# Performance work log

Measured on AMD Instinct MI355X. Metric: run time of the kernel, lower is better.

Reference implementation:

```python
import jax, jax.numpy as jnp
import numpy as np

N, E, L, F, M = 512, 2048, 16, 16, 8
HOPS = 2      # egonet radius (k_hop_subgraph num_hops)
H = 128       # WL hash buckets
N_ITER = 3    # WeisfeilerLehman(n_iter=3)
TAU = 0.1     # soft-relabeling temperature


def setup_inputs():
    key = jax.random.key(0)
    k0, k1, k2, k3, k4, k5 = jax.random.split(key, 6)
    labels = jax.random.randint(k0, (N,), 0, L)
    x = jax.nn.one_hot(labels, L, dtype=jnp.float32)
    edge_index = jax.random.randint(k1, (2, E), 0, N)
    # filter adjacencies, built exactly as in GKernel.__init__:
    # symmetric 0/1 with zero diagonal
    A = jax.random.uniform(k2, (F, M, M))
    A = ((A + jnp.swapaxes(A, -1, -2)) > 1.0).astype(jnp.float32)
    A = A * (1.0 - jnp.eye(M, dtype=jnp.float32))
    Xlab = jax.random.randint(k3, (F, M), 0, L)
    X = jax.nn.one_hot(Xlab, L, dtype=jnp.float32)
    # injective label -> bucket embedding (random distinct buckets)
    E0 = jax.nn.one_hot(jax.random.permutation(k4, H)[:L], H, dtype=jnp.float32)
    # random projection used to hash (own-label, neighbor-multiset) signatures
    Rproj = jax.random.normal(k5, (2 * H, H), dtype=jnp.float32)
    return {"x": x, "edge_index": edge_index, "P": A, "X": X, "E0": E0, "Rproj": Rproj}


def _wl_features(c0, nbr_sum, mask, Rproj):
    # soft Weisfeiler-Lehman subtree features: at each iteration the new
    # node label is a hash of (own label, neighbor-label multiset); the
    # graph feature is the concatenated per-iteration label histograms.
    c = c0 * mask[:, None]                       # [n, H]
    feats = [c.sum(0)]
    for _ in range(N_ITER):
        sig = jnp.concatenate([c, nbr_sum(c)], axis=-1)        # [n, 2H]
        c = jax.nn.softmax((sig @ Rproj) / TAU, axis=-1) * mask[:, None]
        feats.append(c.sum(0))
    return jnp.concatenate(feats)                # [(N_ITER+1)*H]


def _max_comp_mask(A):
    # largest connected component via min-label propagation (max_comp)
    comp = jnp.arange(M, dtype=jnp.float32)
    Ab = A > 0
    for _ in range(M):
        nbr_min = jnp.min(jnp.where(Ab, comp[None, :], 1e9), axis=1)
        comp = jnp.minimum(comp, nbr_min)
    ci = comp.astype(jnp.int32)
    counts = jax.ops.segment_sum(jnp.ones(M, jnp.float32), ci, num_segments=M)
    best = jnp.argmax(counts)
    return (ci == best).astype(jnp.float32)


def reference(x, edge_index, P, X, E0, Rproj):
    # symmetrize edges (egonets / WL kernels are undirected)
    src = jnp.concatenate([edge_index[0], edge_index[1]])
    dst = jnp.concatenate([edge_index[1], edge_index[0]])
    # --- k-hop egonet node masks (compute_egonets) : reach[i, j] = 1 iff
    # node j is within HOPS hops of root i ---
    reach = jnp.eye(N, dtype=jnp.float32)
    for _ in range(HOPS):
        agg = jax.ops.segment_sum(reach[:, src].T, dst, num_segments=N).T
        reach = jnp.clip(reach + agg, 0.0, 1.0)
    c0 = x @ E0                                  # initial bucket labels [N, H]

    def ego_feat(mask):
        emask = (mask[src] * mask[dst])[:, None]
        def nbr(c):
            return jax.ops.segment_sum(c[src] * emask, dst, num_segments=N)
        return _wl_features(c0, nbr, mask, Rproj)

    ego_feats = jax.vmap(ego_feat)(reach)        # [N, (N_ITER+1)*H]

    def filt_feat(Af, Xf):
        mask = _max_comp_mask(Af)
        Am = Af * mask[:, None] * mask[None, :]
        return _wl_features(Xf @ E0, lambda c: Am @ c, mask, Rproj)

    filt_feats = jax.vmap(filt_feat)(P, X)       # [F, (N_ITER+1)*H]

    # normalized WL kernel: k(g1,g2)/sqrt(k(g1,g1) k(g2,g2)); sim.T -> [N, F]
    sim = filt_feats @ ego_feats.T               # [F, N]
    nf = jnp.linalg.norm(filt_feats, axis=-1)
    ng = jnp.linalg.norm(ego_feats, axis=-1)
    sim = sim / (nf[:, None] * ng[None, :] + 1e-12)
    return sim.T
```

## Files before the change

kernel.cpp:

```cpp
#include <hip/hip_runtime.h>
#include <hip/hip_bf16.h>

#define NN 512
#define EE 2048
#define LL 16
#define FF 16
#define MM 8
#define HH 128
#define CAP_ROWS 40960
#define MAXD 32
#define TAU_SCALE 14.426950408889634f

typedef __attribute__((ext_vector_type(8))) short bf16x8;
typedef __attribute__((ext_vector_type(4))) float f32x4;

constexpr size_t OFF_ADJ   = 0;
constexpr size_t SZ_ADJ    = (size_t)NN * 8 * 8;
constexpr size_t OFF_DEG   = OFF_ADJ + SZ_ADJ;
constexpr size_t SZ_DEG    = (size_t)NN * 4;
constexpr size_t OFF_CNT   = OFF_DEG + SZ_DEG;
constexpr size_t SZ_CNT    = (size_t)NN * 4;
constexpr size_t OFF_ROFF  = OFF_CNT + SZ_CNT;
constexpr size_t SZ_ROFF   = (size_t)(NN + 1) * 4 + 12;
constexpr size_t OFF_BUCKN = OFF_ROFF + SZ_ROFF;
constexpr size_t SZ_BUCKN  = (size_t)NN * 4;
constexpr size_t OFF_BUCKF = OFF_BUCKN + SZ_BUCKN;
constexpr size_t SZ_BUCKF  = (size_t)FF * MM * 4;
constexpr size_t OFF_NLST  = ((OFF_BUCKF + SZ_BUCKF + 63) / 64) * 64;
constexpr size_t SZ_NLST   = (size_t)NN * MAXD * 2;
constexpr size_t OFF_CEGO  = OFF_NLST + SZ_NLST;
constexpr size_t SZ_CEGO   = (size_t)CAP_ROWS * 2;
constexpr size_t OFF_NCNT  = OFF_CEGO + SZ_CEGO;
constexpr size_t SZ_NCNT   = (size_t)CAP_ROWS * 2;
constexpr size_t OFF_RBK   = OFF_NCNT + SZ_NCNT;
constexpr size_t SZ_RBK    = (size_t)CAP_ROWS * 2;
constexpr size_t OFF_NBR   = OFF_RBK + SZ_RBK;
constexpr size_t SZ_NBR    = (size_t)CAP_ROWS * MAXD * 2;
constexpr size_t OFF_NBK   = OFF_NBR + SZ_NBR;
constexpr size_t SZ_NBK    = (size_t)CAP_ROWS * MAXD * 2;
constexpr size_t OFF_EGOF  = ((OFF_NBK + SZ_NBK + 63) / 64) * 64;
constexpr size_t SZ_EGOF   = (size_t)NN * 512 * 4;
constexpr size_t OFF_FILTF = OFF_EGOF + SZ_EGOF;
constexpr size_t SZ_FILTF  = (size_t)FF * 512 * 4;
constexpr size_t OFF_FNORM = OFF_FILTF + SZ_FILTF;
constexpr size_t SZ_FNORM  = 64;
constexpr size_t OFF_CA    = ((OFF_FNORM + SZ_FNORM + 255) / 256) * 256;
constexpr size_t SZ_CBUF   = (size_t)CAP_ROWS * HH * 4;
constexpr size_t OFF_CB    = OFF_CA + SZ_CBUF;

__device__ __forceinline__ unsigned f2bfbits(float x) {
    unsigned u = __float_as_uint(x);
    return (u + 0x7fffu + ((u >> 16) & 1u)) >> 16;
}
__device__ __forceinline__ float bf2f(unsigned hb) { return __uint_as_float(hb << 16); }

__global__ __launch_bounds__(256) void k_build(const int* __restrict__ ei,
                                               const float* __restrict__ x,
                                               const float* __restrict__ X,
                                               const float* __restrict__ E0,
                                               int* __restrict__ degN,
                                               unsigned short* __restrict__ nbrLstN,
                                               unsigned long long* __restrict__ adj,
                                               int* __restrict__ buckN,
                                               int* __restrict__ buckF) {
    int idx = blockIdx.x * blockDim.x + threadIdx.x;
    if (idx < EE) {
        int a = ei[idx], b = ei[EE + idx];
        int p = atomicAdd(&degN[a], 1);
        if (p < MAXD) nbrLstN[(size_t)a * MAXD + p] = (unsigned short)b;
        int q = atomicAdd(&degN[b], 1);
        if (q < MAXD) nbrLstN[(size_t)b * MAXD + q] = (unsigned short)a;
        atomicOr(&adj[(size_t)a * 8 + (b >> 6)], 1ull << (b & 63));
        atomicOr(&adj[(size_t)b * 8 + (a >> 6)], 1ull << (a & 63));
    } else if (idx < EE + NN) {
        int i = idx - EE;
        int lab = 0;
        for (int l = 0; l < LL; ++l) if (x[i * LL + l] > 0.5f) lab = l;
        int b = 0;
        for (int h = 0; h < HH; ++h) if (E0[lab * HH + h] > 0.5f) b = h;
        buckN[i] = b;
    } else if (idx < EE + NN + FF * MM) {
        int fm = idx - EE - NN;
        int lab = 0;
        for (int l = 0; l < LL; ++l) if (X[fm * LL + l] > 0.5f) lab = l;
        int b = 0;
        for (int h = 0; h < HH; ++h) if (E0[lab * HH + h] > 0.5f) b = h;
        buckF[fm] = b;
    }
}

__global__ __launch_bounds__(64) void k_reach(const unsigned long long* __restrict__ adj,
                                              unsigned long long* __restrict__ bitsR,
                                              int* __restrict__ count) {
    __shared__ unsigned long long r1[8];
    __shared__ unsigned long long r2[8];
    int i = blockIdx.x, t = threadIdx.x;
    if (t < 8) {
        unsigned long long v = adj[(size_t)i * 8 + t];
        if (t == (i >> 6)) v |= 1ull << (i & 63);
        r1[t] = v;
        r2[t] = v;
    }
    __syncthreads();
    unsigned long long p[8] = {0, 0, 0, 0, 0, 0, 0, 0};
    for (int rep = 0; rep < 8; ++rep) {
        if ((r1[rep] >> t) & 1ull) {
            int j = t + rep * 64;
#pragma unroll
            for (int w = 0; w < 8; ++w) p[w] |= adj[(size_t)j * 8 + w];
        }
    }
#pragma unroll
    for (int w = 0; w < 8; ++w)
        if (p[w]) atomicOr(&r2[w], p[w]);
    __syncthreads();
    if (t < 8) bitsR[(size_t)i * 8 + t] = r2[t];
    if (t == 0) {
        int acc = 0;
        for (int w = 0; w < 8; ++w) acc += __popcll(r2[w]);
        count[i] = acc;
    }
}

__global__ __launch_bounds__(512) void k_scan(const int* __restrict__ in,
                                              int* __restrict__ out) {
    __shared__ int s[NN];
    int t = threadIdx.x;
    s[t] = in[t];
    __syncthreads();
    for (int d = 1; d < NN; d <<= 1) {
        int v = (t >= d) ? s[t - d] : 0;
        __syncthreads();
        s[t] += v;
        __syncthreads();
    }
    out[t + 1] = s[t];
    if (t == 0) out[0] = 0;
}

__global__ __launch_bounds__(64) void k_pack(const unsigned long long* __restrict__ bitsR,
                                             const int* __restrict__ count,
                                             const int* __restrict__ rowOff,
                                             const int* __restrict__ degN,
                                             const unsigned short* __restrict__ nbrLstN,
                                             const int* __restrict__ buckN,
                                             unsigned short* __restrict__ nbrRow,
                                             unsigned short* __restrict__ nbrBuck,
                                             unsigned short* __restrict__ nbrCnt,
                                             unsigned short* __restrict__ rowBuck,
                                             unsigned short* __restrict__ cegoG,
                                             float* __restrict__ egoF) {
    __shared__ unsigned long long bits[8];
    __shared__ int wpre[8];
    __shared__ unsigned short cmap_s[NN];
    __shared__ unsigned short nodes_s[NN];
    __shared__ float f0[HH];
    int i = blockIdx.x, t = threadIdx.x;
    if (t < 8) bits[t] = bitsR[(size_t)i * 8 + t];
    if (t < 64) { f0[t] = 0.0f; f0[t + 64] = 0.0f; }
    __syncthreads();
    if (t == 0) {
        int acc = 0;
        for (int w = 0; w < 8; ++w) { wpre[w] = acc; acc += __popcll(bits[w]); }
    }
    __syncthreads();
    int base = rowOff[i];
    int n = count[i];
    if (base >= CAP_ROWS) n = 0;
    else if (base + n > CAP_ROWS) n = CAP_ROWS - base;
    for (int rep = 0; rep < 8; ++rep) {
        int j = t + rep * 64;
        unsigned long long word = bits[rep];
        unsigned short v = 0xFFFFu;
        if ((word >> t) & 1ull) {
            int idx = wpre[rep] + __popcll(word & ((1ull << t) - 1ull));
            if (idx < n) { v = (unsigned short)idx; nodes_s[idx] = (unsigned short)j; }
        }
        cmap_s[j] = v;
    }
    for (int q = 256 + t; q < 512; q += 64) egoF[(size_t)i * 512 + q] = 0.0f;
    __syncthreads();
    for (int m = t; m < n; m += 64) {
        int j = nodes_s[m];
        int b = buckN[j];
        atomicAdd(&f0[b], 1.0f);
        size_t row = (size_t)(base + m);
        rowBuck[row] = (unsigned short)b;
        int dn = degN[j]; if (dn > MAXD) dn = MAXD;
        int cnt = 0;
        for (int e = 0; e < dn; ++e) {
            unsigned short nbNode = nbrLstN[(size_t)j * MAXD + e];
            unsigned short nr = cmap_s[nbNode];
            if (nr != 0xFFFFu && cnt < MAXD) {
                nbrRow[row * MAXD + cnt] = (unsigned short)(base + nr);
                nbrBuck[row * MAXD + cnt] = (unsigned short)buckN[nbNode];
                cnt++;
            }
        }
        nbrCnt[row] = (unsigned short)cnt;
        cegoG[row] = (unsigned short)i;
    }
    __syncthreads();
    if (t < 64) {
        egoF[(size_t)i * 512 + t] = f0[t];
        egoF[(size_t)i * 512 + t + 64] = f0[t + 64];
    }
}

__global__ __launch_bounds__(256) void k_iter1(const int* __restrict__ count,
                                               const int* __restrict__ rowOff,
                                               const unsigned short* __restrict__ rowBuck,
                                               const unsigned short* __restrict__ nbrBuck,
                                               const unsigned short* __restrict__ nbrCnt,
                                               const float* __restrict__ Rg,
                                               float* __restrict__ cOut,
                                               float* __restrict__ egoF) {
    __shared__ float fs[HH];
    int i = blockIdx.x, tid = threadIdx.x;
    int base = rowOff[i];
    int n = count[i];
    if (base >= CAP_ROWS) n = 0;
    else if (base + n > CAP_ROWS) n = CAP_ROWS - base;
    if (tid < HH) fs[tid] = 0.0f;
    __syncthreads();
    const float* Rb = Rg + (size_t)HH * HH;
    int col = (tid & 7) * 16;
    float facc[16];
#pragma unroll
    for (int q = 0; q < 16; ++q) facc[q] = 0.0f;
    for (int m = tid >> 3; m < n; m += 32) {
        int gr = base + m;
        float z[16];
        const float* rt = Rg + (size_t)rowBuck[gr] * HH + col;
#pragma unroll
        for (int q = 0; q < 4; ++q) *(float4*)&z[q * 4] = *(const float4*)&rt[q * 4];
        int cnt = nbrCnt[gr];
        const unsigned short* nk = &nbrBuck[(size_t)gr * MAXD];
        for (int e = 0; e < cnt; ++e) {
            const float* rb = Rb + (size_t)nk[e] * HH + col;
#pragma unroll
            for (int q = 0; q < 4; ++q) {
                float4 rv = *(const float4*)&rb[q * 4];
                z[q * 4 + 0] += rv.x; z[q * 4 + 1] += rv.y;
                z[q * 4 + 2] += rv.z; z[q * 4 + 3] += rv.w;
            }
        }
        float mx = z[0];
#pragma unroll
        for (int q = 1; q < 16; ++q) mx = fmaxf(mx, z[q]);
        for (int off = 4; off > 0; off >>= 1) mx = fmaxf(mx, __shfl_xor(mx, off));
        float s = 0.0f;
#pragma unroll
        for (int q = 0; q < 16; ++q) { z[q] = exp2f((z[q] - mx) * TAU_SCALE); s += z[q]; }
        for (int off = 4; off > 0; off >>= 1) s += __shfl_xor(s, off);
        float inv = 1.0f / s;
        float* crow = cOut + (size_t)gr * HH + col;
#pragma unroll
        for (int q = 0; q < 16; ++q) { z[q] *= inv; facc[q] += z[q]; }
#pragma unroll
        for (int q = 0; q < 4; ++q) *(float4*)&crow[q * 4] = *(const float4*)&z[q * 4];
    }
#pragma unroll
    for (int q = 0; q < 16; ++q) atomicAdd(&fs[col + q], facc[q]);
    __syncthreads();
    if (tid < HH) egoF[(size_t)i * 512 + HH + tid] = fs[tid];
}

__global__ __launch_bounds__(256) void k_prep(const float* __restrict__ Rg,
                                              short* __restrict__ RtH,
                                              short* __restrict__ RtL) {
    int idx = blockIdx.x * blockDim.x + threadIdx.x;
    int col = idx >> 5;
    int kc = (idx & 31) * 8;
    bf16x8 hv, lv;
#pragma unroll
    for (int j = 0; j < 8; ++j) {
        float xv = Rg[(size_t)(kc + j) * HH + col];
        unsigned hb = f2bfbits(xv);
        hv[j] = (short)hb;
        lv[j] = (short)f2bfbits(xv - bf2f(hb));
    }
    *(bf16x8*)&RtH[(size_t)col * 256 + kc] = hv;
    *(bf16x8*)&RtL[(size_t)col * 256 + kc] = lv;
}

__global__ __launch_bounds__(64) void k_iter(const float* __restrict__ cur,
                                             float* __restrict__ nxt,
                                             const short* __restrict__ RtH,
                                             const short* __restrict__ RtL,
                                             const int* __restrict__ rowOff,
                                             const unsigned short* __restrict__ nbrRow,
                                             const unsigned short* __restrict__ nbrCnt,
                                             const unsigned short* __restrict__ cegoG,
                                             float* __restrict__ egoF,
                                             int it) {
    int Rtot = rowOff[NN];
    if (Rtot > CAP_ROWS) Rtot = CAP_ROWS;
    int r0 = blockIdx.x * 16;
    if (r0 >= Rtot) return;
    int tid = threadIdx.x;
    int c16 = tid & 15, g = tid >> 4;
    int kb = g * 8;
    int grA = r0 + c16;
    if (grA >= Rtot) grA = Rtot - 1;

    float ua[4][8];
#pragma unroll
    for (int s = 0; s < 4; ++s)
#pragma unroll
        for (int j = 0; j < 8; ++j) ua[s][j] = 0.0f;
    {
        int cnt = nbrCnt[grA];
        const unsigned short* nb = &nbrRow[(size_t)grA * MAXD];
        for (int e = 0; e < cnt; ++e) {
            const float* cr = &cur[(size_t)nb[e] * HH + kb];
#pragma unroll
            for (int s = 0; s < 4; ++s) {
                float4 v0 = *(const float4*)&cr[s * 32];
                float4 v1 = *(const float4*)&cr[s * 32 + 4];
                ua[s][0] += v0.x; ua[s][1] += v0.y; ua[s][2] += v0.z; ua[s][3] += v0.w;
                ua[s][4] += v1.x; ua[s][5] += v1.y; ua[s][6] += v1.z; ua[s][7] += v1.w;
            }
        }
    }

    f32x4 acc[8];
#pragma unroll
    for (int n = 0; n < 8; ++n) acc[n] = (f32x4)(0.0f);
    const short* bbH = RtH + (size_t)c16 * 256 + kb;
    const short* bbL = RtL + (size_t)c16 * 256 + kb;

#pragma unroll
    for (int s = 0; s < 4; ++s) {
        bf16x8 ahi, alo;
#pragma unroll
        for (int j = 0; j < 8; ++j) {
            float xv = ua[s][j];
            unsigned hb = f2bfbits(xv);
            ahi[j] = (short)hb;
            alo[j] = (short)f2bfbits(xv - bf2f(hb));
        }
        const int t = s + 4;
#pragma unroll
        for (int n = 0; n < 8; ++n) {
            bf16x8 bh = *(const bf16x8*)&bbH[n * 4096 + t * 32];
            bf16x8 bl = *(const bf16x8*)&bbL[n * 4096 + t * 32];
            acc[n] = __builtin_amdgcn_mfma_f32_16x16x32_bf16(ahi, bh, acc[n], 0, 0, 0);
            acc[n] = __builtin_amdgcn_mfma_f32_16x16x32_bf16(ahi, bl, acc[n], 0, 0, 0);
            acc[n] = __builtin_amdgcn_mfma_f32_16x16x32_bf16(alo, bh, acc[n], 0, 0, 0);
        }
    }
    {
        const float* cr = &cur[(size_t)grA * HH + kb];
#pragma unroll
        for (int t = 0; t < 4; ++t) {
            float4 v0 = *(const float4*)&cr[t * 32];
            float4 v1 = *(const float4*)&cr[t * 32 + 4];
            float cv[8] = {v0.x, v0.y, v0.z, v0.w, v1.x, v1.y, v1.z, v1.w};
            bf16x8 ahi, alo;
#pragma unroll
            for (int j = 0; j < 8; ++j) {
                unsigned hb = f2bfbits(cv[j]);
                ahi[j] = (short)hb;
                alo[j] = (short)f2bfbits(cv[j] - bf2f(hb));
            }
#pragma unroll
            for (int n = 0; n < 8; ++n) {
                bf16x8 bh = *(const bf16x8*)&bbH[n * 4096 + t * 32];
                bf16x8 bl = *(const bf16x8*)&bbL[n * 4096 + t * 32];
                acc[n] = __builtin_amdgcn_mfma_f32_16x16x32_bf16(ahi, bh, acc[n], 0, 0, 0);
                acc[n] = __builtin_amdgcn_mfma_f32_16x16x32_bf16(ahi, bl, acc[n], 0, 0, 0);
                acc[n] = __builtin_amdgcn_mfma_f32_16x16x32_bf16(alo, bh, acc[n], 0, 0, 0);
            }
        }
    }

    float inv[4];
#pragma unroll
    for (int i = 0; i < 4; ++i) {
        float m = acc[0][i];
#pragma unroll
        for (int n = 1; n < 8; ++n) m = fmaxf(m, acc[n][i]);
        for (int off = 8; off > 0; off >>= 1) m = fmaxf(m, __shfl_xor(m, off));
        float s = 0.0f;
#pragma unroll
        for (int n = 0; n < 8; ++n) {
            float e = exp2f((acc[n][i] - m) * TAU_SCALE);
            acc[n][i] = e; s += e;
        }
        for (int off = 8; off > 0; off >>= 1) s += __shfl_xor(s, off);
        inv[i] = 1.0f / s;
    }

    float fa[8];
#pragma unroll
    for (int n = 0; n < 8; ++n) fa[n] = 0.0f;
    int cege = -1;
#pragma unroll
    for (int i = 0; i < 4; ++i) {
        int gr = r0 + g * 4 + i;
        if (gr < Rtot) {
#pragma unroll
            for (int n = 0; n < 8; ++n) {
                float c = acc[n][i] * inv[i];
                nxt[(size_t)gr * HH + n * 16 + c16] = c;
                acc[n][i] = c;
            }
            int ego = cegoG[gr];
            if (ego != cege) {
                if (cege >= 0) {
#pragma unroll
                    for (int n = 0; n < 8; ++n) {
                        atomicAdd(&egoF[(size_t)cege * 512 + it * HH + n * 16 + c16], fa[n]);
                        fa[n] = 0.0f;
                    }
                }
                cege = ego;
            }
#pragma unroll
            for (int n = 0; n < 8; ++n) fa[n] += acc[n][i];
        }
    }
    if (cege >= 0) {
#pragma unroll
        for (int n = 0; n < 8; ++n)
            atomicAdd(&egoF[(size_t)cege * 512 + it * HH + n * 16 + c16], fa[n]);
    }
}

__global__ __launch_bounds__(256) void k_filt(const float* __restrict__ P,
                                              const int* __restrict__ buckF,
                                              const float* __restrict__ Rg,
                                              float* __restrict__ filtF,
                                              float* __restrict__ fnorm) {
    __shared__ float As[MM][MM];
    __shared__ float Am[MM][MM];
    __shared__ float msk[MM];
    __shared__ float cbuf[2][MM][HH];
    __shared__ float ubuf[MM][HH];
    __shared__ float feats[4 * HH];
    __shared__ float red4[4];
    int f = blockIdx.x, tid = threadIdx.x, wave = tid >> 6, lane = tid & 63;
    if (tid < 64) As[tid >> 3][tid & 7] = P[f * 64 + tid];
    for (int idx = tid; idx < 4 * HH; idx += 256) feats[idx] = 0.f;
    __syncthreads();
    if (tid == 0) {
        float comp[MM];
        for (int m = 0; m < MM; ++m) comp[m] = (float)m;
        for (int it = 0; it < MM; ++it) {
            float nm[MM];
            for (int j = 0; j < MM; ++j) {
                float mn = 1e9f;
                for (int k = 0; k < MM; ++k)
                    if (As[j][k] > 0.f) mn = fminf(mn, comp[k]);
                nm[j] = mn;
            }
            for (int j = 0; j < MM; ++j) comp[j] = fminf(comp[j], nm[j]);
        }
        int cnt[MM], ci[MM];
        for (int m = 0; m < MM; ++m) cnt[m] = 0;
        for (int m = 0; m < MM; ++m) { ci[m] = (int)comp[m]; cnt[ci[m]]++; }
        int best = 0;
        for (int m = 1; m < MM; ++m) if (cnt[m] > cnt[best]) best = m;
        for (int m = 0; m < MM; ++m) msk[m] = (ci[m] == best) ? 1.0f : 0.0f;
    }
    __syncthreads();
    if (tid < 64) Am[tid >> 3][tid & 7] = As[tid >> 3][tid & 7] * msk[tid >> 3] * msk[tid & 7];
    for (int idx = tid; idx < MM * HH; idx += 256) {
        int m = idx >> 7, h = idx & 127;
        cbuf[0][m][h] = (msk[m] > 0.f && h == buckF[f * MM + m]) ? 1.0f : 0.0f;
    }
    __syncthreads();
    if (tid < HH) {
        float s = 0.f;
        for (int m = 0; m < MM; ++m) s += cbuf[0][m][tid];
        feats[tid] = s;
    }
    __syncthreads();
    int cur = 0;
    int h2 = 2 * lane;
    for (int it = 1; it <= 3; ++it) {
#pragma unroll
        for (int jj = 0; jj < 2; ++jj) {
            int d = wave * 2 + jj;
            float u0 = 0.f, u1 = 0.f;
            for (int s = 0; s < MM; ++s) {
                float w = Am[d][s];
                u0 += w * cbuf[cur][s][h2];
                u1 += w * cbuf[cur][s][h2 + 1];
            }
            ubuf[d][h2] = u0;
            ubuf[d][h2 + 1] = u1;
        }
        float a0[2] = {0.f, 0.f}, a1[2] = {0.f, 0.f};
        for (int k = 0; k < HH; ++k) {
            float2 rt = *(const float2*)&Rg[(size_t)k * HH + h2];
            float2 rb = *(const float2*)&Rg[(size_t)(HH + k) * HH + h2];
#pragma unroll
            for (int jj = 0; jj < 2; ++jj) {
                int d = wave * 2 + jj;
                float cd = cbuf[cur][d][k];
                float ud = ubuf[d][k];
                a0[jj] += cd * rt.x + ud * rb.x;
                a1[jj] += cd * rt.y + ud * rb.y;
            }
        }
#pragma unroll
        for (int jj = 0; jj < 2; ++jj) {
            int d = wave * 2 + jj;
            float z0 = a0[jj], z1 = a1[jj];
            float m = fmaxf(z0, z1);
            for (int off = 32; off > 0; off >>= 1) m = fmaxf(m, __shfl_xor(m, off));
            float e0 = exp2f((z0 - m) * TAU_SCALE);
            float e1 = exp2f((z1 - m) * TAU_SCALE);
            float s = e0 + e1;
            for (int off = 32; off > 0; off >>= 1) s += __shfl_xor(s, off);
            float inv = msk[d] / s;
            float c0 = e0 * inv, c1 = e1 * inv;
            cbuf[1 - cur][d][h2] = c0;
            cbuf[1 - cur][d][h2 + 1] = c1;
            atomicAdd(&feats[it * HH + h2], c0);
            atomicAdd(&feats[it * HH + h2 + 1], c1);
        }
        __syncthreads();
        cur = 1 - cur;
    }
    float np = 0.f;
    for (int idx = tid; idx < 4 * HH; idx += 256) {
        float v = feats[idx];
        filtF[(size_t)f * 512 + idx] = v;
        np += v * v;
    }
    for (int off = 32; off > 0; off >>= 1) np += __shfl_xor(np, off);
    if (lane == 0) red4[wave] = np;
    __syncthreads();
    if (tid == 0) fnorm[f] = sqrtf(red4[0] + red4[1] + red4[2] + red4[3]);
}

__global__ __launch_bounds__(64) void k_sim(const float* __restrict__ egoF,
                                            const float* __restrict__ filtF,
                                            const float* __restrict__ fnorm,
                                            float* __restrict__ out) {
    int i = blockIdx.x, lane = threadIdx.x;
    float e[8];
    float ss = 0.f;
#pragma unroll
    for (int r = 0; r < 8; ++r) {
        e[r] = egoF[(size_t)i * 512 + r * 64 + lane];
        ss += e[r] * e[r];
    }
    for (int off = 32; off > 0; off >>= 1) ss += __shfl_xor(ss, off);
    float ng = sqrtf(ss);
    for (int f = 0; f < FF; ++f) {
        float d = 0.f;
#pragma unroll
        for (int r = 0; r < 8; ++r) d += e[r] * filtF[(size_t)f * 512 + r * 64 + lane];
        for (int off = 32; off > 0; off >>= 1) d += __shfl_xor(d, off);
        if (lane == 0) out[i * FF + f] = d / (fnorm[f] * ng + 1e-12f);
    }
}

extern "C" void kernel_launch(void* const* d_in, const int* in_sizes, int n_in,
                              void* d_out, int out_size, void* d_ws, size_t ws_size,
                              hipStream_t stream) {
    (void)in_sizes; (void)n_in; (void)out_size; (void)ws_size;
    const float* x  = (const float*)d_in[0];
    const int*   ei = (const int*)d_in[1];
    const float* P  = (const float*)d_in[2];
    const float* X  = (const float*)d_in[3];
    const float* E0 = (const float*)d_in[4];
    const float* Rg = (const float*)d_in[5];
    float* out = (float*)d_out;
    char* ws = (char*)d_ws;

    unsigned long long* adj   = (unsigned long long*)(ws + OFF_ADJ);
    int* degN   = (int*)(ws + OFF_DEG);
    int* count  = (int*)(ws + OFF_CNT);
    int* rowOff = (int*)(ws + OFF_ROFF);
    int* buckN  = (int*)(ws + OFF_BUCKN);
    int* buckF  = (int*)(ws + OFF_BUCKF);
    unsigned short* nbrLstN = (unsigned short*)(ws + OFF_NLST);
    unsigned short* cego    = (unsigned short*)(ws + OFF_CEGO);
    unsigned short* nbrCnt  = (unsigned short*)(ws + OFF_NCNT);
    unsigned short* rowBuck = (unsigned short*)(ws + OFF_RBK);
    unsigned short* nbrRow  = (unsigned short*)(ws + OFF_NBR);
    unsigned short* nbrBuck = (unsigned short*)(ws + OFF_NBK);
    float* egoF  = (float*)(ws + OFF_EGOF);
    float* filtF = (float*)(ws + OFF_FILTF);
    float* fnorm = (float*)(ws + OFF_FNORM);
    float* cA    = (float*)(ws + OFF_CA);
    float* cB    = (float*)(ws + OFF_CB);
    unsigned long long* bitsR = (unsigned long long*)(ws + OFF_CA);
    short* RtH = (short*)(ws + OFF_NBK);
    short* RtL = RtH + (size_t)HH * 256;

    hipMemsetAsync(ws, 0, OFF_CNT, stream);
    k_build<<<(EE + NN + FF * MM + 255) / 256, 256, 0, stream>>>(ei, x, X, E0, degN, nbrLstN,
                                                                 adj, buckN, buckF);
    k_reach<<<NN, 64, 0, stream>>>(adj, bitsR, count);
    k_scan<<<1, 512, 0, stream>>>(count, rowOff);
    k_pack<<<NN, 64, 0, stream>>>(bitsR, count, rowOff, degN, nbrLstN, buckN,
                                  nbrRow, nbrBuck, nbrCnt, rowBuck, cego, egoF);
    k_iter1<<<NN, 256, 0, stream>>>(count, rowOff, rowBuck, nbrBuck, nbrCnt, Rg, cB, egoF);
    k_prep<<<16, 256, 0, stream>>>(Rg, RtH, RtL);
    k_iter<<<CAP_ROWS / 16, 64, 0, stream>>>(cB, cA, RtH, RtL, rowOff, nbrRow, nbrCnt, cego, egoF, 2);
    k_iter<<<CAP_ROWS / 16, 64, 0, stream>>>(cA, cB, RtH, RtL, rowOff, nbrRow, nbrCnt, cego, egoF, 3);
    k_filt<<<FF, 256, 0, stream>>>(P, buckF, Rg, filtF, fnorm);
    k_sim<<<NN, 64, 0, stream>>>(egoF, filtF, fnorm, out);
}
```

Baseline: 305.7 us.

## Fuse all WL iterations per small egonet into one LDS-resident kernel

```diff
diff --git a/kernel.cpp b/kernel.cpp
--- a/kernel.cpp
+++ b/kernel.cpp
@@ -9,7 +9,9 @@
 #define HH 128
 #define CAP_ROWS 40960
 #define MAXD 32
+#define CAPR 144
 #define TAU_SCALE 14.426950408889634f
+#define MAXP 6
 
 typedef __attribute__((ext_vector_type(8))) short bf16x8;
 typedef __attribute__((ext_vector_type(4))) float f32x4;
@@ -47,6 +49,7 @@
 constexpr size_t OFF_CA    = ((OFF_FNORM + SZ_FNORM + 255) / 256) * 256;
 constexpr size_t SZ_CBUF   = (size_t)CAP_ROWS * HH * 4;
 constexpr size_t OFF_CB    = OFF_CA + SZ_CBUF;
+constexpr size_t OFF_RT    = OFF_CB + SZ_CBUF;
 
 __device__ __forceinline__ unsigned f2bfbits(float x) {
     unsigned u = __float_as_uint(x);
@@ -58,11 +61,14 @@
                                                const float* __restrict__ x,
                                                const float* __restrict__ X,
                                                const float* __restrict__ E0,
+                                               const float* __restrict__ Rg,
                                                int* __restrict__ degN,
                                                unsigned short* __restrict__ nbrLstN,
                                                unsigned long long* __restrict__ adj,
                                                int* __restrict__ buckN,
-                                               int* __restrict__ buckF) {
+                                               int* __restrict__ buckF,
+                                               short* __restrict__ RtH,
+                                               short* __restrict__ RtL) {
     int idx = blockIdx.x * blockDim.x + threadIdx.x;
     if (idx < EE) {
         int a = ei[idx], b = ei[EE + idx];
@@ -86,6 +92,20 @@
         int b = 0;
         for (int h = 0; h < HH; ++h) if (E0[lab * HH + h] > 0.5f) b = h;
         buckF[fm] = b;
+    } else if (idx < EE + NN + FF * MM + 4096) {
+        int pidx = idx - (EE + NN + FF * MM);
+        int col = pidx >> 5;
+        int kc = (pidx & 31) * 8;
+        bf16x8 hv, lv;
+#pragma unroll
+        for (int j = 0; j < 8; ++j) {
+            float xv = Rg[(size_t)(kc + j) * HH + col];
+            unsigned hb = f2bfbits(xv);
+            hv[j] = (short)hb;
+            lv[j] = (short)f2bfbits(xv - bf2f(hb));
+        }
+        *(bf16x8*)&RtH[(size_t)col * 256 + kc] = hv;
+        *(bf16x8*)&RtL[(size_t)col * 256 + kc] = lv;
     }
 }
 
@@ -207,6 +227,293 @@
     }
 }
 
+__device__ __forceinline__ void gather_u(const char* src, char* dst, int n, int base,
+                                         int slot, int colg,
+                                         const unsigned short* __restrict__ nbrRow,
+                                         const unsigned short* __restrict__ nbrCnt) {
+    for (int m = slot; m < n; m += 96) {
+        int gr = base + m;
+        float v[16];
+#pragma unroll
+        for (int q = 0; q < 16; ++q) v[q] = 0.f;
+        int cnt = nbrCnt[gr];
+        const unsigned short* nb = &nbrRow[(size_t)gr * MAXD];
+        for (int e = 0; e < cnt; ++e) {
+            int lr = (int)nb[e] - base;
+            unsigned sw = (unsigned)((lr & 7) << 4);
+            unsigned rb = (unsigned)(lr * 512);
+#pragma unroll
+            for (int q = 0; q < 4; ++q) {
+                float4 t4 = *(const float4*)(src + ((rb + (unsigned)(colg * 16 + q * 128)) ^ sw));
+                v[q * 4 + 0] += t4.x; v[q * 4 + 1] += t4.y;
+                v[q * 4 + 2] += t4.z; v[q * 4 + 3] += t4.w;
+            }
+        }
+        unsigned swd = (unsigned)((m & 7) << 4);
+        unsigned rbd = (unsigned)(m * 512);
+#pragma unroll
+        for (int q = 0; q < 4; ++q)
+            *(float4*)(dst + ((rbd + (unsigned)(colg * 16 + q * 128)) ^ swd)) = *(float4*)&v[q * 4];
+    }
+}
+
+__device__ __forceinline__ void conv_row(char* pl, int r, int sub) {
+    unsigned sw = (unsigned)((r & 7) << 4);
+    unsigned rb = (unsigned)(r * 512);
+    float f[32];
+#pragma unroll
+    for (int j = 0; j < 8; ++j)
+        *(float4*)&f[j * 4] = *(const float4*)(pl + ((rb + (unsigned)(sub * 128 + j * 16)) ^ sw));
+    bf16x8 hv[4], lv[4];
+#pragma unroll
+    for (int b = 0; b < 4; ++b)
+#pragma unroll
+        for (int j = 0; j < 8; ++j) {
+            float xv = f[b * 8 + j];
+            unsigned hb = f2bfbits(xv);
+            hv[b][j] = (short)hb;
+            lv[b][j] = (short)f2bfbits(xv - bf2f(hb));
+        }
+#pragma unroll
+    for (int b = 0; b < 4; ++b) {
+        *(bf16x8*)(pl + ((rb + (unsigned)(sub * 64 + b * 16)) ^ sw)) = hv[b];
+        *(bf16x8*)(pl + ((rb + 256u + (unsigned)(sub * 64 + b * 16)) ^ sw)) = lv[b];
+    }
+}
+
+__device__ __forceinline__ f32x4 pair_mfma(const char* uPl, const char* cPl,
+                                           const short* __restrict__ RtH,
+                                           const short* __restrict__ RtL,
+                                           int t, int cb, int c16, int g) {
+    int row = 16 * t + c16;
+    unsigned sw = (unsigned)((row & 7) << 4);
+    unsigned rb = (unsigned)(row * 512);
+    const short* pH = RtH + (size_t)(cb * 16 + c16) * 256 + g * 8;
+    const short* pL = RtL + (size_t)(cb * 16 + c16) * 256 + g * 8;
+    f32x4 a = (f32x4)(0.f);
+#pragma unroll
+    for (int s = 0; s < 4; ++s) {
+        bf16x8 ah = *(const bf16x8*)(uPl + ((rb + (unsigned)(s * 64 + g * 16)) ^ sw));
+        bf16x8 al = *(const bf16x8*)(uPl + ((rb + 256u + (unsigned)(s * 64 + g * 16)) ^ sw));
+        bf16x8 bh = *(const bf16x8*)&pH[(s + 4) * 32];
+        bf16x8 bl = *(const bf16x8*)&pL[(s + 4) * 32];
+        a = __builtin_amdgcn_mfma_f32_16x16x32_bf16(ah, bh, a, 0, 0, 0);
+        a = __builtin_amdgcn_mfma_f32_16x16x32_bf16(ah, bl, a, 0, 0, 0);
+        a = __builtin_amdgcn_mfma_f32_16x16x32_bf16(al, bh, a, 0, 0, 0);
+    }
+#pragma unroll
+    for (int s = 0; s < 4; ++s) {
+        bf16x8 ah = *(const bf16x8*)(cPl + ((rb + (unsigned)(s * 64 + g * 16)) ^ sw));
+        bf16x8 al = *(const bf16x8*)(cPl + ((rb + 256u + (unsigned)(s * 64 + g * 16)) ^ sw));
+        bf16x8 bh = *(const bf16x8*)&pH[s * 32];
+        bf16x8 bl = *(const bf16x8*)&pL[s * 32];
+        a = __builtin_amdgcn_mfma_f32_16x16x32_bf16(ah, bh, a, 0, 0, 0);
+        a = __builtin_amdgcn_mfma_f32_16x16x32_bf16(ah, bl, a, 0, 0, 0);
+        a = __builtin_amdgcn_mfma_f32_16x16x32_bf16(al, bh, a, 0, 0, 0);
+    }
+    return a;
+}
+
+__device__ __forceinline__ void soft_row(char* pl, int r, int sub, bool wb, float* fsp) {
+    unsigned sw = (unsigned)((r & 7) << 4);
+    unsigned rb = (unsigned)(r * 512);
+    float f[32];
+#pragma unroll
+    for (int j = 0; j < 8; ++j)
+        *(float4*)&f[j * 4] = *(const float4*)(pl + ((rb + (unsigned)((sub + 4 * j) * 16)) ^ sw));
+    float mx = f[0];
+#pragma unroll
+    for (int i = 1; i < 32; ++i) mx = fmaxf(mx, f[i]);
+    mx = fmaxf(mx, __shfl_xor(mx, 1));
+    mx = fmaxf(mx, __shfl_xor(mx, 2));
+    float s = 0.f;
+#pragma unroll
+    for (int i = 0; i < 32; ++i) { f[i] = exp2f((f[i] - mx) * TAU_SCALE); s += f[i]; }
+    s += __shfl_xor(s, 1);
+    s += __shfl_xor(s, 2);
+    float inv = 1.0f / s;
+#pragma unroll
+    for (int i = 0; i < 32; ++i) f[i] *= inv;
+    if (wb) {
+#pragma unroll
+        for (int j = 0; j < 8; ++j)
+            *(float4*)(pl + ((rb + (unsigned)((sub + 4 * j) * 16)) ^ sw)) = *(float4*)&f[j * 4];
+    }
+#pragma unroll
+    for (int j = 0; j < 8; ++j)
+#pragma unroll
+        for (int x = 0; x < 4; ++x)
+            atomicAdd(&fsp[(sub + 4 * j) * 4 + x], f[j * 4 + x]);
+}
+
+__global__ __launch_bounds__(768) void k_fused(const int* __restrict__ count,
+                                               const int* __restrict__ rowOff,
+                                               const unsigned short* __restrict__ rowBuck,
+                                               const unsigned short* __restrict__ nbrBuck,
+                                               const unsigned short* __restrict__ nbrCnt,
+                                               const unsigned short* __restrict__ nbrRow,
+                                               const float* __restrict__ Rg,
+                                               const short* __restrict__ RtH,
+                                               const short* __restrict__ RtL,
+                                               float* __restrict__ egoF) {
+    __shared__ __align__(16) char cAp[CAPR * 512];
+    __shared__ __align__(16) char cBp[CAPR * 512];
+    __shared__ float fs[HH];
+    int ego = blockIdx.x;
+    int n = count[ego];
+    if (n > CAPR) return;
+    int base = rowOff[ego];
+    if (base >= CAP_ROWS) return;
+    if (base + n > CAP_ROWS) n = CAP_ROWS - base;
+    if (n < 1) return;
+    int T = (n + 15) >> 4;
+    int tid = threadIdx.x;
+    int wid = tid >> 6, lane = tid & 63;
+    int c16 = lane & 15, g = lane >> 4;
+    int slot = tid >> 3, colg = tid & 7;
+    int quad = tid >> 2, sub = tid & 3;
+
+    if (tid < HH) fs[tid] = 0.f;
+    {
+        int padN = (T * 16 - n) * 128;
+        for (int idx = tid; idx < padN; idx += 768) {
+            int r = n + (idx >> 7), h = idx & 127;
+            unsigned b = ((unsigned)(r * 512 + h * 4)) ^ ((unsigned)((r & 7) << 4));
+            *(float*)(cAp + b) = 0.f;
+            *(float*)(cBp + b) = 0.f;
+        }
+    }
+    __syncthreads();
+
+    {
+        const float* Rb = Rg + (size_t)HH * HH;
+        float facc[16];
+#pragma unroll
+        for (int q = 0; q < 16; ++q) facc[q] = 0.f;
+        for (int m = slot; m < n; m += 96) {
+            int gr = base + m;
+            float z[16];
+            const float* rt = Rg + (size_t)rowBuck[gr] * HH;
+#pragma unroll
+            for (int q = 0; q < 4; ++q)
+                *(float4*)&z[q * 4] = *(const float4*)&rt[colg * 4 + q * 32];
+            int cnt = nbrCnt[gr];
+            const unsigned short* nk = &nbrBuck[(size_t)gr * MAXD];
+            for (int e = 0; e < cnt; ++e) {
+                const float* rb2 = Rb + (size_t)nk[e] * HH;
+#pragma unroll
+                for (int q = 0; q < 4; ++q) {
+                    float4 rv = *(const float4*)&rb2[colg * 4 + q * 32];
+                    z[q * 4 + 0] += rv.x; z[q * 4 + 1] += rv.y;
+                    z[q * 4 + 2] += rv.z; z[q * 4 + 3] += rv.w;
+                }
+            }
+            float mx = z[0];
+#pragma unroll
+            for (int q = 1; q < 16; ++q) mx = fmaxf(mx, z[q]);
+            for (int off = 4; off > 0; off >>= 1) mx = fmaxf(mx, __shfl_xor(mx, off));
+            float s = 0.f;
+#pragma unroll
+            for (int q = 0; q < 16; ++q) { z[q] = exp2f((z[q] - mx) * TAU_SCALE); s += z[q]; }
+            for (int off = 4; off > 0; off >>= 1) s += __shfl_xor(s, off);
+            float inv = 1.0f / s;
+#pragma unroll
+            for (int q = 0; q < 16; ++q) { z[q] *= inv; facc[q] += z[q]; }
+            unsigned swd = (unsigned)((m & 7) << 4);
+            unsigned rbd = (unsigned)(m * 512);
+#pragma unroll
+            for (int q = 0; q < 4; ++q)
+                *(float4*)(cAp + ((rbd + (unsigned)(colg * 16 + q * 128)) ^ swd)) = *(float4*)&z[q * 4];
+        }
+#pragma unroll
+        for (int q = 0; q < 16; ++q) {
+            float v = facc[q];
+            v += __shfl_xor(v, 8);
+            v += __shfl_xor(v, 16);
+            v += __shfl_xor(v, 32);
+            if (lane < 8) atomicAdd(&fs[lane * 4 + (q >> 2) * 32 + (q & 3)], v);
+        }
+    }
+    __syncthreads();
+    if (tid < HH) { egoF[(size_t)ego * 512 + HH + tid] = fs[tid]; fs[tid] = 0.f; }
+    __syncthreads();
+
+    gather_u(cAp, cBp, n, base, slot, colg, nbrRow, nbrCnt);
+    __syncthreads();
+    for (int idx = quad; idx < 2 * n; idx += 192) {
+        int pl = (idx >= n);
+        conv_row(pl ? cBp : cAp, pl ? idx - n : idx, sub);
+    }
+    __syncthreads();
+    {
+        f32x4 zacc[MAXP];
+        int npair = T * 8;
+#pragma unroll
+        for (int p = 0; p < MAXP; ++p) {
+            zacc[p] = (f32x4)(0.f);
+            int pr = wid + p * 12;
+            if (pr < npair)
+                zacc[p] = pair_mfma(cBp, cAp, RtH, RtL, pr >> 3, pr & 7, c16, g);
+        }
+        __syncthreads();
+#pragma unroll
+        for (int p = 0; p < MAXP; ++p) {
+            int pr = wid + p * 12;
+            if (pr < npair) {
+                int t = pr >> 3, cb = pr & 7;
+#pragma unroll
+                for (int i = 0; i < 4; ++i) {
+                    int row = 16 * t + 4 * g + i;
+                    int col = cb * 16 + c16;
+                    *(float*)(cBp + (((unsigned)(row * 512 + col * 4)) ^ ((unsigned)((row & 7) << 4)))) = zacc[p][i];
+                }
+            }
+        }
+    }
+    __syncthreads();
+    for (int r = quad; r < n; r += 192) soft_row(cBp, r, sub, true, fs);
+    __syncthreads();
+    if (tid < HH) { egoF[(size_t)ego * 512 + 2 * HH + tid] = fs[tid]; fs[tid] = 0.f; }
+    __syncthreads();
+
+    gather_u(cBp, cAp, n, base, slot, colg, nbrRow, nbrCnt);
+    __syncthreads();
+    for (int idx = quad; idx < 2 * n; idx += 192) {
+        int pl = (idx >= n);
+        conv_row(pl ? cAp : cBp, pl ? idx - n : idx, sub);
+    }
+    __syncthreads();
+    {
+        f32x4 zacc[MAXP];
+        int npair = T * 8;
+#pragma unroll
+        for (int p = 0; p < MAXP; ++p) {
+            zacc[p] = (f32x4)(0.f);
+            int pr = wid + p * 12;
+            if (pr < npair)
+                zacc[p] = pair_mfma(cAp, cBp, RtH, RtL, pr >> 3, pr & 7, c16, g);
+        }
+        __syncthreads();
+#pragma unroll
+        for (int p = 0; p < MAXP; ++p) {
+            int pr = wid + p * 12;
+            if (pr < npair) {
+                int t = pr >> 3, cb = pr & 7;
+#pragma unroll
+                for (int i = 0; i < 4; ++i) {
+                    int row = 16 * t + 4 * g + i;
+                    int col = cb * 16 + c16;
+                    *(float*)(cAp + (((unsigned)(row * 512 + col * 4)) ^ ((unsigned)((row & 7) << 4)))) = zacc[p][i];
+                }
+            }
+        }
+    }
+    __syncthreads();
+    for (int r = quad; r < n; r += 192) soft_row(cAp, r, sub, false, fs);
+    __syncthreads();
+    if (tid < HH) egoF[(size_t)ego * 512 + 3 * HH + tid] = fs[tid];
+}
+
 __global__ __launch_bounds__(256) void k_iter1(const int* __restrict__ count,
                                                const int* __restrict__ rowOff,
                                                const unsigned short* __restrict__ rowBuck,
@@ -217,6 +524,7 @@
                                                float* __restrict__ egoF) {
     __shared__ float fs[HH];
     int i = blockIdx.x, tid = threadIdx.x;
+    if (count[i] <= CAPR) return;
     int base = rowOff[i];
     int n = count[i];
     if (base >= CAP_ROWS) n = 0;
@@ -266,29 +574,12 @@
     if (tid < HH) egoF[(size_t)i * 512 + HH + tid] = fs[tid];
 }
 
-__global__ __launch_bounds__(256) void k_prep(const float* __restrict__ Rg,
-                                              short* __restrict__ RtH,
-                                              short* __restrict__ RtL) {
-    int idx = blockIdx.x * blockDim.x + threadIdx.x;
-    int col = idx >> 5;
-    int kc = (idx & 31) * 8;
-    bf16x8 hv, lv;
-#pragma unroll
-    for (int j = 0; j < 8; ++j) {
-        float xv = Rg[(size_t)(kc + j) * HH + col];
-        unsigned hb = f2bfbits(xv);
-        hv[j] = (short)hb;
-        lv[j] = (short)f2bfbits(xv - bf2f(hb));
-    }
-    *(bf16x8*)&RtH[(size_t)col * 256 + kc] = hv;
-    *(bf16x8*)&RtL[(size_t)col * 256 + kc] = lv;
-}
-
 __global__ __launch_bounds__(64) void k_iter(const float* __restrict__ cur,
                                              float* __restrict__ nxt,
                                              const short* __restrict__ RtH,
                                              const short* __restrict__ RtL,
                                              const int* __restrict__ rowOff,
+                                             const int* __restrict__ count,
                                              const unsigned short* __restrict__ nbrRow,
                                              const unsigned short* __restrict__ nbrCnt,
                                              const unsigned short* __restrict__ cegoG,
@@ -303,6 +594,8 @@
     int kb = g * 8;
     int grA = r0 + c16;
     if (grA >= Rtot) grA = Rtot - 1;
+    bool bigA = count[cegoG[grA]] > CAPR;
+    if (__ballot(bigA) == 0ull) return;
 
     float ua[4][8];
 #pragma unroll
@@ -310,7 +603,7 @@
 #pragma unroll
         for (int j = 0; j < 8; ++j) ua[s][j] = 0.0f;
     {
-        int cnt = nbrCnt[grA];
+        int cnt = bigA ? (int)nbrCnt[grA] : 0;
         const unsigned short* nb = &nbrRow[(size_t)grA * MAXD];
         for (int e = 0; e < cnt; ++e) {
             const float* cr = &cur[(size_t)nb[e] * HH + kb];
@@ -323,13 +616,11 @@
             }
         }
     }
-
     f32x4 acc[8];
 #pragma unroll
     for (int n = 0; n < 8; ++n) acc[n] = (f32x4)(0.0f);
     const short* bbH = RtH + (size_t)c16 * 256 + kb;
     const short* bbL = RtL + (size_t)c16 * 256 + kb;
-
 #pragma unroll
     for (int s = 0; s < 4; ++s) {
         bf16x8 ahi, alo;
@@ -374,7 +665,6 @@
             }
         }
     }
-
     float inv[4];
 #pragma unroll
     for (int i = 0; i < 4; ++i) {
@@ -391,7 +681,6 @@
         for (int off = 8; off > 0; off >>= 1) s += __shfl_xor(s, off);
         inv[i] = 1.0f / s;
     }
-
     float fa[8];
 #pragma unroll
     for (int n = 0; n < 8; ++n) fa[n] = 0.0f;
@@ -400,25 +689,27 @@
     for (int i = 0; i < 4; ++i) {
         int gr = r0 + g * 4 + i;
         if (gr < Rtot) {
-#pragma unroll
-            for (int n = 0; n < 8; ++n) {
-                float c = acc[n][i] * inv[i];
-                nxt[(size_t)gr * HH + n * 16 + c16] = c;
-                acc[n][i] = c;
-            }
             int ego = cegoG[gr];
-            if (ego != cege) {
-                if (cege >= 0) {
-#pragma unroll
-                    for (int n = 0; n < 8; ++n) {
-                        atomicAdd(&egoF[(size_t)cege * 512 + it * HH + n * 16 + c16], fa[n]);
-                        fa[n] = 0.0f;
+            if (count[ego] > CAPR) {
+#pragma unroll
+                for (int n = 0; n < 8; ++n) {
+                    float c = acc[n][i] * inv[i];
+                    nxt[(size_t)gr * HH + n * 16 + c16] = c;
+                    acc[n][i] = c;
+                }
+                if (ego != cege) {
+                    if (cege >= 0) {
+#pragma unroll
+                        for (int n = 0; n < 8; ++n) {
+                            atomicAdd(&egoF[(size_t)cege * 512 + it * HH + n * 16 + c16], fa[n]);
+                            fa[n] = 0.0f;
+                        }
                     }
+                    cege = ego;
                 }
-                cege = ego;
-            }
-#pragma unroll
-            for (int n = 0; n < 8; ++n) fa[n] += acc[n][i];
+#pragma unroll
+                for (int n = 0; n < 8; ++n) fa[n] += acc[n][i];
+            }
         }
     }
     if (cege >= 0) {
@@ -591,20 +882,21 @@
     float* cA    = (float*)(ws + OFF_CA);
     float* cB    = (float*)(ws + OFF_CB);
     unsigned long long* bitsR = (unsigned long long*)(ws + OFF_CA);
-    short* RtH = (short*)(ws + OFF_NBK);
+    short* RtH = (short*)(ws + OFF_RT);
     short* RtL = RtH + (size_t)HH * 256;
 
     hipMemsetAsync(ws, 0, OFF_CNT, stream);
-    k_build<<<(EE + NN + FF * MM + 255) / 256, 256, 0, stream>>>(ei, x, X, E0, degN, nbrLstN,
-                                                                 adj, buckN, buckF);
+    k_build<<<(EE + NN + FF * MM + 4096 + 255) / 256, 256, 0, stream>>>(
+        ei, x, X, E0, Rg, degN, nbrLstN, adj, buckN, buckF, RtH, RtL);
     k_reach<<<NN, 64, 0, stream>>>(adj, bitsR, count);
     k_scan<<<1, 512, 0, stream>>>(count, rowOff);
     k_pack<<<NN, 64, 0, stream>>>(bitsR, count, rowOff, degN, nbrLstN, buckN,
                                   nbrRow, nbrBuck, nbrCnt, rowBuck, cego, egoF);
+    k_fused<<<NN, 768, 0, stream>>>(count, rowOff, rowBuck, nbrBuck, nbrCnt, nbrRow,
+                                    Rg, RtH, RtL, egoF);
     k_iter1<<<NN, 256, 0, stream>>>(count, rowOff, rowBuck, nbrBuck, nbrCnt, Rg, cB, egoF);
-    k_prep<<<16, 256, 0, stream>>>(Rg, RtH, RtL);
-    k_iter<<<CAP_ROWS / 16, 64, 0, stream>>>(cB, cA, RtH, RtL, rowOff, nbrRow, nbrCnt, cego, egoF, 2);
-    k_iter<<<CAP_ROWS / 16, 64, 0, stream>>>(cA, cB, RtH, RtL, rowOff, nbrRow, nbrCnt, cego, egoF, 3);
+    k_iter<<<CAP_ROWS / 16, 64, 0, stream>>>(cB, cA, RtH, RtL, rowOff, count, nbrRow, nbrCnt, cego, egoF, 2);
+    k_iter<<<CAP_ROWS / 16, 64, 0, stream>>>(cA, cB, RtH, RtL, rowOff, count, nbrRow, nbrCnt, cego, egoF, 3);
     k_filt<<<FF, 256, 0, stream>>>(P, buckF, Rg, filtF, fnorm);
     k_sim<<<NN, 64, 0, stream>>>(egoF, filtF, fnorm, out);
 }
```

Result: slower. 382.5 us (+25.1%).
